# Kernel tuning notes

Hardware: AMD Instinct MI355X
Metric: run time of the kernel (lower is better)

The kernel has to match this reference:

```python
import jax, jax.numpy as jnp
import numpy as np

B, H, W, C, NB = 3, 256, 256, 16, 4
EPS = 1e-3  # keras BatchNormalization default epsilon


def _conv(x, w, b):
    y = jax.lax.conv_general_dilated(x, w, (1, 1), 'SAME',
                                     dimension_numbers=('NHWC', 'HWIO', 'NHWC'))
    return y + b


def _bn(x, g, be, mu, v):
    # inference-mode batch norm with moving statistics
    return (x - mu) * jax.lax.rsqrt(v + EPS) * g + be


def _extract_patches(x, p, s):
    # tf.image.extract_patches(..., padding='SAME') -> (b, oh, ow, p, p, c)
    b, h, w, c = x.shape
    oh, ow = -(-h // s), -(-w // s)
    pth = max((oh - 1) * s + p - h, 0)
    ptw = max((ow - 1) * s + p - w, 0)
    xp = jnp.pad(x, ((0, 0), (pth // 2, pth - pth // 2), (ptw // 2, ptw - ptw // 2), (0, 0)))
    ri = np.arange(oh)[:, None] * s + np.arange(p)[None, :]  # (oh, p)
    ci = np.arange(ow)[:, None] * s + np.arange(p)[None, :]  # (ow, p)
    return xp[:, ri[:, None, :, None], ci[None, :, None, :], :]


def setup_inputs() -> dict:
    key = jax.random.key(0)
    ks = jax.random.split(key, 4)
    mr = jax.random.normal(ks[0], (B, H, W, C), jnp.float32)
    pet = jax.random.normal(ks[1], (B, H, W, C), jnp.float32)
    W1 = jax.random.normal(ks[2], (3, 3, C, C * NB), jnp.float32) * 0.05
    W2 = jax.random.normal(ks[3], (3, 3, C * NB, C * NB), jnp.float32) * 0.05
    z = jnp.zeros((C * NB,), jnp.float32)
    o = jnp.ones((C * NB,), jnp.float32)
    return dict(mr_features=mr, pet_features=pet,
                W1=W1, b1=z, g1=o, be1=z, mu1=z, v1=o,
                W2=W2, b2=z, g2=o, be2=z, mu2=z, v2=o,
                patch=8, stride=4)


def reference(mr_features, pet_features, W1, b1, g1, be1, mu1, v1,
              W2, b2, g2, be2, mu2, v2, patch, stride):
    px = py = int(patch)
    sx = sy = int(stride)
    bsz, h, w, c = mr_features.shape

    # ---- B_Kernel_Function_Generator ----
    x = jax.nn.relu(_bn(_conv(mr_features, W1, b1), g1, be1, mu1, v1))
    x = _bn(_conv(x, W2, b2), g2, be2, mu2, v2)  # last conv_block: no activation
    nb = x.shape[-1] // c
    x = x.reshape(bsz, h, w, c, nb)
    x = jax.nn.softmax(x, axis=-1)
    b_features = jnp.where(x > 1e-5, x, 0.0)  # mask * x

    # ---- Sparse_Kernel_Matrix_Multiplication ----
    bc, bf = c, nb
    Nx, Ny = h // px, w // py
    lx, ly = px // sx, py // sy
    SNx, SNy = Nx * lx, Ny * ly

    bflat = b_features.reshape(bsz, h, w, bc * bf)
    bp = _extract_patches(bflat, px, sx).reshape(bsz, SNx, SNy, px, py, bc, bf)
    pp = _extract_patches(pet_features, px, sx).reshape(bsz, SNx, SNy, px, py, bc, 1)

    dn = jnp.sum(bp, axis=(3, 4), keepdims=True)              # diagonal norm
    kp = jnp.sum(pp * bp, axis=(3, 4), keepdims=True)         # kernel-weighted PET
    dn_safe = jnp.where(dn == 0, 1.0, dn)
    kn = jnp.where(dn == 0, 0.0, kp / dn_safe) * bp           # divide_no_nan
    kpet = jnp.sum(kn, axis=-1)                               # (b,SNx,SNy,px,py,bc)

    # deinterleave stride phases: kernel_pet[:, i::lx, j::ly] stack
    kp6 = kpet.reshape(bsz, Nx, lx, Ny, ly, px, py, c)
    st = kp6.transpose(4, 2, 0, 1, 3, 5, 6, 7).reshape(lx * ly, bsz, Nx, Ny, px, py, c)
    t = st.transpose(1, 2, 3, 4, 5, 6, 0).reshape(bsz, Nx, Ny, px, py, c, lx, ly)
    t = t.transpose(0, 1, 3, 2, 4, 5, 6, 7).reshape(bsz, Nx * px, Ny * py, c, lx, ly)
    t = t.transpose(4, 5, 0, 1, 2, 3)  # (lx, ly, b, H, W, c)

    # align_patches: roll each shifted copy back into registration, then mean
    rev = t.transpose(2, 3, 4, 5, 0, 1).reshape(bsz, h, w, c, lx * ly)
    rev = rev.transpose(4, 0, 1, 2, 3)  # (lx*ly, b, H, W, c)
    rollx = np.arange(-px // 2 + sx // 2, px // 2 + sx // 2, sx)
    rolly = np.arange(-py // 2 + sy // 2, py // 2 + sy // 2, sy)
    acc = jnp.zeros((bsz, h, w, c), rev.dtype)
    for m in range(lx * ly):  # small fixed set (lx*ly = 4)
        acc = acc + jnp.roll(rev[m], (int(rollx[m % lx]), int(rolly[m // lx])), axis=(1, 2))
    return acc / (lx * ly)
```

## Files before the change

### kernel.cpp

```cpp
#include <hip/hip_runtime.h>

#define EPSB 1e-3f

typedef _Float16 half8 __attribute__((ext_vector_type(8)));
typedef _Float16 half4 __attribute__((ext_vector_type(4)));
typedef float f32x4 __attribute__((ext_vector_type(4)));

__global__ __launch_bounds__(256, 4)
void k_prep(const float* __restrict__ W1, const float* __restrict__ W2,
            const float* __restrict__ b1, const float* __restrict__ g1,
            const float* __restrict__ be1, const float* __restrict__ mu1,
            const float* __restrict__ v1,
            const float* __restrict__ b2, const float* __restrict__ g2,
            const float* __restrict__ be2, const float* __restrict__ mu2,
            const float* __restrict__ v2,
            _Float16* __restrict__ W1F, _Float16* __restrict__ W2F,
            float* __restrict__ ST)
{
    int t = blockIdx.x * 256 + threadIdx.x;
    if (t < 5 * 4 * 64 * 8) {
        int k = t & 7, lane = (t >> 3) & 63, snt = t >> 9;
        int s = snt >> 2, ct = snt & 3;
        int quad = lane >> 4, n16 = lane & 15;
        int tap = 2 * s + (quad >> 1);
        int ci  = (quad & 1) * 8 + k;
        int co  = ct * 16 + n16;
        float v = (tap < 9) ? W1[(tap * 16 + ci) * 64 + co] : 0.f;
        W1F[t] = (_Float16)v;
        return;
    }
    t -= 5 * 4 * 64 * 8;
    if (t < 18 * 4 * 64 * 8) {
        int k = t & 7, lane = (t >> 3) & 63, snt = t >> 9;
        int s = snt >> 2, ct = snt & 3;
        int quad = lane >> 4, n16 = lane & 15;
        int tap = s >> 1;
        int ci  = (s & 1) * 32 + quad * 8 + k;
        int co  = ct * 16 + n16;
        W2F[t] = (_Float16)W2[(tap * 64 + ci) * 64 + co];
        return;
    }
    t -= 18 * 4 * 64 * 8;
    if (t < 256) {
        int c = t & 63, sel = t >> 6;
        if (sel == 0)      ST[c]       = g1[c] * rsqrtf(v1[c] + EPSB);
        else if (sel == 1) ST[64 + c]  = (b1[c] - mu1[c]) * (g1[c] * rsqrtf(v1[c] + EPSB)) + be1[c];
        else if (sel == 2) ST[128 + c] = g2[c] * rsqrtf(v2[c] + EPSB);
        else               ST[192 + c] = (b2[c] - mu2[c]) * (g2[c] * rsqrtf(v2[c] + EPSB)) + be2[c];
    }
}

#define CIPM 20
#define CIP2 72
__global__ __launch_bounds__(256, 3)
void k_convf(const float* __restrict__ mr, const _Float16* __restrict__ W1F,
             const _Float16* __restrict__ W2F, const float* __restrict__ ST,
             const float* __restrict__ pet,
             _Float16* __restrict__ BF, float* __restrict__ S2)
{
    __shared__ __align__(16) _Float16 sMR[6 * 68 * CIPM];
    __shared__ __align__(16) _Float16 sC1[4 * 66 * 64];
    const int tid = threadIdx.x;
    const int b  = blockIdx.y;
    const int r0 = (blockIdx.x >> 2) * 2;
    const int q0 = (blockIdx.x & 3) * 64;

    for (int idx = tid; idx < 6 * 68 * 2; idx += 256) {
        int c = idx & 1, pp = idx >> 1;
        int p = pp % 68, dys = pp / 68;
        int rr = r0 + dys - 2, qg = q0 + p - 2;
        half8 h = (half8)(_Float16)0.f;
        if ((unsigned)rr < 256u && (unsigned)qg < 256u) {
            const float* src = mr + ((b * 256 + rr) * 256 + qg) * 16 + c * 8;
            float4 v0 = *(const float4*)src;
            float4 v1 = *(const float4*)(src + 4);
            h = (half8){(_Float16)v0.x, (_Float16)v0.y, (_Float16)v0.z, (_Float16)v0.w,
                        (_Float16)v1.x, (_Float16)v1.y, (_Float16)v1.z, (_Float16)v1.w};
        }
        *(half8*)(&sMR[pp * CIPM + c * 8]) = h;
    }
    __syncthreads();

    const int w = tid >> 6, lane = tid & 63;
    const int n16 = lane & 15, quad = lane >> 4;

    {
        const _Float16* Wl1 = W1F + lane * 8;
        const int ci0 = (quad & 1) * 8;
        #pragma unroll
        for (int k = 0; k < 5; ++k) {
            const int g  = w + 4 * k;
            const int y  = g / 5;
            const int xi = g % 5;
            const int x0 = xi * 13 - ((xi >> 2) << 1);
            const int px = x0 + n16;

            f32x4 a1[4];
            #pragma unroll
            for (int ct = 0; ct < 4; ++ct) a1[ct] = (f32x4){0.f, 0.f, 0.f, 0.f};

            half8 wf1[2][4], pf1[2];
            auto load1 = [&](int s, int buf) {
                int tap  = 2 * s + (quad >> 1);
                int tapc = tap > 8 ? 8 : tap;
                int dy = tapc / 3, dx = tapc % 3;
                #pragma unroll
                for (int ct = 0; ct < 4; ++ct)
                    wf1[buf][ct] = *(const half8*)(Wl1 + (s * 4 + ct) * 512);
                pf1[buf] = *(const half8*)&sMR[((y + dy) * 68 + px + dx) * CIPM + ci0];
            };
            load1(0, 0);
            load1(1, 1);
            #pragma unroll
            for (int s = 0; s < 5; ++s) {
                const int buf = s & 1;
                #pragma unroll
                for (int ct = 0; ct < 4; ++ct)
                    a1[ct] = __builtin_amdgcn_mfma_f32_16x16x32_f16(wf1[buf][ct], pf1[buf], a1[ct], 0, 0, 0);
                if (s + 2 < 5) load1(s + 2, buf);
            }

            const bool valid = ((unsigned)(r0 - 1 + y) < 256u) && ((unsigned)(q0 - 1 + px) < 256u);
            #pragma unroll
            for (int ct = 0; ct < 4; ++ct) {
                int co0 = ct * 16 + quad * 4;
                f32x4 sc = *(const f32x4*)&ST[co0];
                f32x4 sh = *(const f32x4*)&ST[64 + co0];
                half4 h;
                #pragma unroll
                for (int j = 0; j < 4; ++j)
                    h[j] = (_Float16)fmaxf(a1[ct][j] * sc[j] + sh[j], 0.f);
                if (!valid) h = (half4)(_Float16)0.f;
                int slot = ct * 2 + (quad >> 1);
                *(half4*)&sC1[(y * 66 + px) * 64 + ((slot ^ (px & 7)) << 3) + (quad & 1) * 4] = h;
            }
        }
    }
    __syncthreads();

    const int row = w >> 1;
    const int qh  = (w & 1) * 32;
    const _Float16* Wl = W2F + lane * 8;

    f32x4 acc[2][4];
    #pragma unroll
    for (int i = 0; i < 2; ++i)
        #pragma unroll
        for (int j = 0; j < 4; ++j) acc[i][j] = (f32x4){0.f, 0.f, 0.f, 0.f};

    half8 wf[3][4], pf[3][2];
    auto load_s = [&](int s, int buf) {
        const int tap = s >> 1;
        const int dy = tap / 3, dx = tap % 3;
        const int slot = (s & 1) * 4 + quad;
        const int sxm = (n16 + dx) & 7;
        #pragma unroll
        for (int ct = 0; ct < 4; ++ct)
            wf[buf][ct] = *(const half8*)(Wl + (s * 4 + ct) * 512);
        #pragma unroll
        for (int qt = 0; qt < 2; ++qt)
            pf[buf][qt] = *(const half8*)&sC1[((row + dy) * 66 + qh + qt * 16 + n16 + dx) * 64 + ((slot ^ sxm) << 3)];
    };
    load_s(0, 0);
    load_s(1, 1);
    load_s(2, 2);
    #pragma unroll
    for (int s = 0; s < 18; ++s) {
        const int buf = s % 3;
        #pragma unroll
        for (int qt = 0; qt < 2; ++qt)
            #pragma unroll
            for (int ct = 0; ct < 4; ++ct)
                acc[qt][ct] = __builtin_amdgcn_mfma_f32_16x16x32_f16(wf[buf][ct], pf[buf][qt], acc[qt][ct], 0, 0, 0);
        if (s + 3 < 18) load_s(s + 3, buf);
    }

    half4 hv[4][2];
    #pragma unroll
    for (int ct = 0; ct < 4; ++ct) {
        int co0 = ct * 16 + quad * 4;
        f32x4 sc = *(const f32x4*)&ST[128 + co0];
        f32x4 sh = *(const f32x4*)&ST[192 + co0];
        #pragma unroll
        for (int qt = 0; qt < 2; ++qt) {
            float z0 = acc[qt][ct][0] * sc[0] + sh[0];
            float z1 = acc[qt][ct][1] * sc[1] + sh[1];
            float z2 = acc[qt][ct][2] * sc[2] + sh[2];
            float z3 = acc[qt][ct][3] * sc[3] + sh[3];
            float mx = fmaxf(fmaxf(z0, z1), fmaxf(z2, z3));
            float e0 = __expf(z0 - mx), e1 = __expf(z1 - mx);
            float e2 = __expf(z2 - mx), e3 = __expf(z3 - mx);
            float inv = __builtin_amdgcn_rcpf((e0 + e1) + (e2 + e3));
            float p0 = e0 * inv, p1 = e1 * inv, p2 = e2 * inv, p3 = e3 * inv;
            half4 h;
            h[0] = (_Float16)(p0 > 1e-5f ? p0 : 0.f);
            h[1] = (_Float16)(p1 > 1e-5f ? p1 : 0.f);
            h[2] = (_Float16)(p2 > 1e-5f ? p2 : 0.f);
            h[3] = (_Float16)(p3 > 1e-5f ? p3 : 0.f);
            hv[ct][qt] = h;
        }
    }
    __syncthreads();
    #pragma unroll
    for (int ct = 0; ct < 4; ++ct) {
        int co0 = ct * 16 + quad * 4;
        #pragma unroll
        for (int qt = 0; qt < 2; ++qt) {
            int ql = qh + qt * 16 + n16;
            *(half4*)(&sC1[(row * 64 + ql) * CIP2 + co0]) = hv[ct][qt];
        }
    }
    __syncthreads();

    for (int idx = tid; idx < 1024; idx += 256) {
        int rl2 = idx >> 9, rest = idx & 511;
        int ql = rest >> 3, seg = rest & 7;
        int4 v = *(const int4*)&sC1[(rl2 * 64 + ql) * CIP2 + seg * 8];
        *(int4*)(BF + (((b * 256 + r0 + rl2) * 256 + q0 + ql) * 64 + seg * 8)) = v;
    }

    const int qp = tid >> 3, chg = tid & 7;
    {
        float dn[8], kp[8];
        #pragma unroll
        for (int j = 0; j < 8; ++j) { dn[j] = 0.f; kp[j] = 0.f; }
        #pragma unroll
        for (int u = 0; u < 2; ++u)
            #pragma unroll
            for (int v = 0; v < 2; ++v) {
                int rl = u, ql = 2 * qp + v;
                half8 bf = *(const half8*)(&sC1[(rl * 64 + ql) * CIP2 + chg * 8]);
                float2 p2 = *(const float2*)(pet + ((b * 256 + r0 + rl) * 256 + q0 + ql) * 16 + chg * 2);
                #pragma unroll
                for (int j = 0; j < 8; ++j) {
                    float bv = (float)bf[j];
                    dn[j] += bv;
                    kp[j] = fmaf((j < 4) ? p2.x : p2.y, bv, kp[j]);
                }
            }
        float* o = S2 + 2 * ((size_t)(((b * 128 + (r0 >> 1)) * 128 + (q0 >> 1) + qp) * 64) + chg * 8);
        #pragma unroll
        for (int m = 0; m < 4; ++m)
            *(float4*)(o + 4 * m) = make_float4(dn[2*m], kp[2*m], dn[2*m+1], kp[2*m+1]);
    }
}

__global__ __launch_bounds__(256, 4)
void k_ratio(const float* __restrict__ S2, float* __restrict__ RATIO)
{
    int t = blockIdx.x * 256 + threadIdx.x;
    int cf = t & 63;
    int j  = (t >> 6) & 63;
    int i  = (t >> 12) & 63;
    int b  = t >> 18;
    float dn = 0.f, kp = 0.f;
    #pragma unroll
    for (int u = 0; u < 4; ++u) {
        int r2 = 2 * i - 1 + u;
        if ((unsigned)r2 >= 128u) continue;
        #pragma unroll
        for (int v = 0; v < 4; ++v) {
            int q2 = 2 * j - 1 + v;
            if ((unsigned)q2 >= 128u) continue;
            float2 s = *(const float2*)(S2 + 2 * (((b * 128 + r2) * 128 + q2) * 64 + cf));
            dn += s.x;
            kp += s.y;
        }
    }
    RATIO[t] = (dn == 0.f) ? 0.f : 0.25f * kp * __builtin_amdgcn_rcpf(dn);
}

__global__ __launch_bounds__(256, 4)
void k_out(const _Float16* __restrict__ BF, const float* __restrict__ RATIO,
           float* __restrict__ out)
{
    __shared__ __align__(16) float sU[64 * 68];
    const int tid = threadIdx.x;
    const int r = blockIdx.x & 255;
    const int b = blockIdx.x >> 8;

    const int i0 = (r <= 253) ? 2 * ((r + 2) >> 3)       : -1;
    const int i1 = (r >= 2)   ? 2 * ((r - 2) >> 3) + 1   : -1;

    for (int idx = tid; idx < 1024; idx += 256) {
        int j = idx >> 4, c4 = idx & 15;
        float4 a = make_float4(0.f, 0.f, 0.f, 0.f);
        if (i0 >= 0) a = *(const float4*)&RATIO[(((b * 64 + i0) * 64 + j) << 6) + 4 * c4];
        float4 bb = make_float4(0.f, 0.f, 0.f, 0.f);
        if (i1 >= 0) bb = *(const float4*)&RATIO[(((b * 64 + i1) * 64 + j) << 6) + 4 * c4];
        *(float4*)&sU[j * 68 + 4 * c4] = make_float4(a.x + bb.x, a.y + bb.y, a.z + bb.z, a.w + bb.w);
    }
    __syncthreads();

    const int q = tid;
    const int j0 = (q <= 253) ? 2 * ((q + 2) >> 3)     : -1;
    const int j1 = (q >= 2)   ? 2 * ((q - 2) >> 3) + 1 : -1;

    const half8* bfp = (const half8*)(BF + ((size_t)(b * 256 + r) * 256 + q) * 64);
    float o[16];
    #pragma unroll
    for (int c = 0; c < 16; ++c) o[c] = 0.f;

    #pragma unroll
    for (int c2 = 0; c2 < 8; ++c2) {
        half8 bf8 = bfp[c2];
        float s0 = 0.f, s1 = 0.f;
        #pragma unroll
        for (int pj = 0; pj < 2; ++pj) {
            int jj = pj ? j1 : j0;
            if (jj < 0) continue;
            const float* up = &sU[jj * 68 + 8 * c2];
            s0 += (float)bf8[0] * up[0] + (float)bf8[1] * up[1]
                + (float)bf8[2] * up[2] + (float)bf8[3] * up[3];
            s1 += (float)bf8[4] * up[4] + (float)bf8[5] * up[5]
                + (float)bf8[6] * up[6] + (float)bf8[7] * up[7];
        }
        o[2 * c2]     = s0;
        o[2 * c2 + 1] = s1;
    }
    float* op = out + ((size_t)(b * 256 + r) * 256 + q) * 16;
    #pragma unroll
    for (int m = 0; m < 4; ++m)
        *(float4*)(op + 4 * m) = make_float4(o[4*m], o[4*m+1], o[4*m+2], o[4*m+3]);
}

extern "C" void kernel_launch(void* const* d_in, const int* in_sizes, int n_in,
                              void* d_out, int out_size, void* d_ws, size_t ws_size,
                              hipStream_t stream) {
    const float* mr  = (const float*)d_in[0];
    const float* pet = (const float*)d_in[1];
    const float* W1  = (const float*)d_in[2];
    const float* b1  = (const float*)d_in[3];
    const float* g1  = (const float*)d_in[4];
    const float* be1 = (const float*)d_in[5];
    const float* mu1 = (const float*)d_in[6];
    const float* v1  = (const float*)d_in[7];
    const float* W2  = (const float*)d_in[8];
    const float* b2  = (const float*)d_in[9];
    const float* g2  = (const float*)d_in[10];
    const float* be2 = (const float*)d_in[11];
    const float* mu2 = (const float*)d_in[12];
    const float* v2  = (const float*)d_in[13];

    char* ws = (char*)d_ws;
    _Float16* BF    = (_Float16*)(ws);
    float*    S2    = (float*)(ws + 25165824);
    float*    RATIO = (float*)(ws + 50331648);
    _Float16* W1F   = (_Float16*)(ws + 53477376);
    _Float16* W2F   = (_Float16*)(ws + 53497856);
    float*    ST    = (float*)(ws + 53571584);
    float*    out   = (float*)d_out;

    dim3 blk(256);
    k_prep<<<185, blk, 0, stream>>>(W1, W2, b1, g1, be1, mu1, v1,
                                    b2, g2, be2, mu2, v2, W1F, W2F, ST);
    k_convf<<<dim3(512, 3), blk, 0, stream>>>(mr, W1F, W2F, ST, pet, BF, S2);
    k_ratio<<<3072, blk, 0, stream>>>(S2, RATIO);
    k_out<<<768, blk, 0, stream>>>(BF, RATIO, out);
}
```

Measured before the change: 170.4 us.

## Split conv2 MFMA work across warps by output-channel tile instead of pixel rows

Conv2 used to give each of the four warps one row-half of pixels and all four output-channel tiles. Now each warp owns one 16-channel tile and covers every pixel of the block (2 rows x 64 columns). Each warp loads only its own weight fragment per step, in a 4-deep register buffer, and reads more activation fragments from LDS (8 per step, 2-deep buffer). This cuts global/L2 weight traffic per warp but raises LDS reads and register pressure for the patch buffers.

```diff
diff --git a/kernel.cpp b/kernel.cpp
--- a/kernel.cpp
+++ b/kernel.cpp
@@ -138,8 +138,7 @@
     }
     __syncthreads();
 
-    const int row = w >> 1;
-    const int qh  = (w & 1) * 32;
+    const int ctw = w;
     const _Float16* Wl = W2F + lane * 8;
 
     f32x4 acc[2][4];
@@ -148,67 +147,72 @@
         #pragma unroll
         for (int j = 0; j < 4; ++j) acc[i][j] = (f32x4){0.f, 0.f, 0.f, 0.f};
 
-    half8 wf[3][4], pf[3][2];
-    auto load_s = [&](int s, int buf) {
+    half8 wfb[4];
+    half8 pfb[2][2][4];
+    auto loadw = [&](int s, int buf) {
+        wfb[buf] = *(const half8*)(Wl + (s * 4 + ctw) * 512);
+    };
+    auto loadp = [&](int s, int buf) {
         const int tap = s >> 1;
         const int dy = tap / 3, dx = tap % 3;
         const int slot = (s & 1) * 4 + quad;
         const int sxm = (n16 + dx) & 7;
         #pragma unroll
-        for (int ct = 0; ct < 4; ++ct)
-            wf[buf][ct] = *(const half8*)(Wl + (s * 4 + ct) * 512);
-        #pragma unroll
-        for (int qt = 0; qt < 2; ++qt)
-            pf[buf][qt] = *(const half8*)&sC1[((row + dy) * 66 + qh + qt * 16 + n16 + dx) * 64 + ((slot ^ sxm) << 3)];
+        for (int rr = 0; rr < 2; ++rr)
+            #pragma unroll
+            for (int qt = 0; qt < 4; ++qt)
+                pfb[buf][rr][qt] = *(const half8*)&sC1[((rr + dy) * 66 + qt * 16 + n16 + dx) * 64 + ((slot ^ sxm) << 3)];
     };
-    load_s(0, 0);
-    load_s(1, 1);
-    load_s(2, 2);
+    loadw(0, 0); loadw(1, 1); loadw(2, 2); loadw(3, 3);
+    loadp(0, 0); loadp(1, 1);
     #pragma unroll
     for (int s = 0; s < 18; ++s) {
-        const int buf = s % 3;
-        #pragma unroll
-        for (int qt = 0; qt < 2; ++qt)
-            #pragma unroll
-            for (int ct = 0; ct < 4; ++ct)
-                acc[qt][ct] = __builtin_amdgcn_mfma_f32_16x16x32_f16(wf[buf][ct], pf[buf][qt], acc[qt][ct], 0, 0, 0);
-        if (s + 3 < 18) load_s(s + 3, buf);
-    }
-
-    half4 hv[4][2];
-    #pragma unroll
-    for (int ct = 0; ct < 4; ++ct) {
-        int co0 = ct * 16 + quad * 4;
+        const int bw = s & 3, bp = s & 1;
+        #pragma unroll
+        for (int rr = 0; rr < 2; ++rr)
+            #pragma unroll
+            for (int qt = 0; qt < 4; ++qt)
+                acc[rr][qt] = __builtin_amdgcn_mfma_f32_16x16x32_f16(wfb[bw], pfb[bp][rr][qt], acc[rr][qt], 0, 0, 0);
+        if (s + 4 < 18) loadw(s + 4, bw);
+        if (s + 2 < 18) loadp(s + 2, bp);
+    }
+
+    half4 hv[2][4];
+    {
+        const int co0 = ctw * 16 + quad * 4;
         f32x4 sc = *(const f32x4*)&ST[128 + co0];
         f32x4 sh = *(const f32x4*)&ST[192 + co0];
         #pragma unroll
-        for (int qt = 0; qt < 2; ++qt) {
-            float z0 = acc[qt][ct][0] * sc[0] + sh[0];
-            float z1 = acc[qt][ct][1] * sc[1] + sh[1];
-            float z2 = acc[qt][ct][2] * sc[2] + sh[2];
-            float z3 = acc[qt][ct][3] * sc[3] + sh[3];
-            float mx = fmaxf(fmaxf(z0, z1), fmaxf(z2, z3));
-            float e0 = __expf(z0 - mx), e1 = __expf(z1 - mx);
-            float e2 = __expf(z2 - mx), e3 = __expf(z3 - mx);
-            float inv = __builtin_amdgcn_rcpf((e0 + e1) + (e2 + e3));
-            float p0 = e0 * inv, p1 = e1 * inv, p2 = e2 * inv, p3 = e3 * inv;
-            half4 h;
-            h[0] = (_Float16)(p0 > 1e-5f ? p0 : 0.f);
-            h[1] = (_Float16)(p1 > 1e-5f ? p1 : 0.f);
-            h[2] = (_Float16)(p2 > 1e-5f ? p2 : 0.f);
-            h[3] = (_Float16)(p3 > 1e-5f ? p3 : 0.f);
-            hv[ct][qt] = h;
-        }
-    }
-    __syncthreads();
-    #pragma unroll
-    for (int ct = 0; ct < 4; ++ct) {
-        int co0 = ct * 16 + quad * 4;
-        #pragma unroll
-        for (int qt = 0; qt < 2; ++qt) {
-            int ql = qh + qt * 16 + n16;
-            *(half4*)(&sC1[(row * 64 + ql) * CIP2 + co0]) = hv[ct][qt];
-        }
+        for (int rr = 0; rr < 2; ++rr)
+            #pragma unroll
+            for (int qt = 0; qt < 4; ++qt) {
+                float z0 = acc[rr][qt][0] * sc[0] + sh[0];
+                float z1 = acc[rr][qt][1] * sc[1] + sh[1];
+                float z2 = acc[rr][qt][2] * sc[2] + sh[2];
+                float z3 = acc[rr][qt][3] * sc[3] + sh[3];
+                float mx = fmaxf(fmaxf(z0, z1), fmaxf(z2, z3));
+                float e0 = __expf(z0 - mx), e1 = __expf(z1 - mx);
+                float e2 = __expf(z2 - mx), e3 = __expf(z3 - mx);
+                float inv = __builtin_amdgcn_rcpf((e0 + e1) + (e2 + e3));
+                float p0 = e0 * inv, p1 = e1 * inv, p2 = e2 * inv, p3 = e3 * inv;
+                half4 h;
+                h[0] = (_Float16)(p0 > 1e-5f ? p0 : 0.f);
+                h[1] = (_Float16)(p1 > 1e-5f ? p1 : 0.f);
+                h[2] = (_Float16)(p2 > 1e-5f ? p2 : 0.f);
+                h[3] = (_Float16)(p3 > 1e-5f ? p3 : 0.f);
+                hv[rr][qt] = h;
+            }
+    }
+    __syncthreads();
+    {
+        const int co0 = ctw * 16 + quad * 4;
+        #pragma unroll
+        for (int rr = 0; rr < 2; ++rr)
+            #pragma unroll
+            for (int qt = 0; qt < 4; ++qt) {
+                int ql = qt * 16 + n16;
+                *(half4*)(&sC1[(rr * 64 + ql) * CIP2 + co0]) = hv[rr][qt];
+            }
     }
     __syncthreads();
 
```

After: 166.2 us. 2.5% less time.
